# Optimization experiments

Hardware: AMD Instinct MI355X
Metric: run time of the kernel (lower is better)

## Reference

```python
import jax, jax.numpy as jnp
import numpy as np

D_MODEL = 256
N_LAYERS = 8
NUM_CLASSES = 3
INPUT_DIM = 1
BATCH = 8
SEQ = 2048
EXIT_IDX = (1, 3, 5, 7)  # n_layers//4-1, n_layers//2-1, 3n//4-1, n-1
LN_EPS = 1e-5


def setup_inputs() -> dict:
    key = jax.random.key(0)
    ks = jax.random.split(key, 16)
    d, nl, nc = D_MODEL, N_LAYERS, NUM_CLASSES
    return {
        "x": jax.random.normal(ks[0], (BATCH, SEQ, INPUT_DIM), jnp.float32),
        "in_W": jax.random.normal(ks[1], (d, INPUT_DIM), jnp.float32) * 0.02,
        "in_b": jnp.zeros((d,), jnp.float32),
        "A_params": jax.random.normal(ks[2], (nl, d), jnp.float32) * 0.1,
        "B_params": jax.random.normal(ks[3], (nl, d), jnp.float32),
        "C_params": jax.random.normal(ks[4], (nl, d), jnp.float32),
        "D_params": jax.random.normal(ks[5], (nl, d), jnp.float32),
        "proj_W": jax.random.normal(ks[6], (nl, d, d), jnp.float32) * 0.02,
        "proj_b": jnp.zeros((nl, d), jnp.float32),
        "ln_g": jnp.ones((nl, d), jnp.float32),
        "ln_b": jnp.zeros((nl, d), jnp.float32),
        "head_W": jax.random.normal(ks[7], (4, nc, d), jnp.float32) * 0.02,
        "head_b": jnp.zeros((4, nc), jnp.float32),
    }


def _ssm_block(x, Ap, Bp, Cp, Dp, pW, pb, g, b):
    # x: [B, L, d]
    Bsz, L, d = x.shape
    A = jax.nn.sigmoid(Ap)                               # [d]
    t = jnp.arange(L, dtype=jnp.float32)
    K = (Cp[:, None] * (A[:, None] ** t[None, :]) * Bp[:, None])[:, None, :]  # [d,1,L]
    xt = jnp.swapaxes(x, 1, 2)                           # [B, d, L]
    # torch F.conv1d(pad=L-1, groups=d) then [..., :L] == left-pad-only cross-correlation
    out = jax.lax.conv_general_dilated(
        xt, K, window_strides=(1,), padding=[(L - 1, 0)], feature_group_count=d
    )                                                    # [B, d, L]
    out = out + Dp[None, :, None] * xt
    out = jnp.swapaxes(out, 1, 2)                        # [B, L, d]
    out = jax.nn.gelu(out, approximate=False) @ pW.T + pb
    y = x + out
    mu = jnp.mean(y, axis=-1, keepdims=True)
    var = jnp.var(y, axis=-1, keepdims=True)
    return (y - mu) / jnp.sqrt(var + LN_EPS) * g + b


def reference(x, in_W, in_b, A_params, B_params, C_params, D_params,
              proj_W, proj_b, ln_g, ln_b, head_W, head_b):
    h = x @ in_W.T + in_b                                # [B, L, d]
    logits = []
    head = 0
    for i in range(N_LAYERS):
        h = _ssm_block(h, A_params[i], B_params[i], C_params[i], D_params[i],
                       proj_W[i], proj_b[i], ln_g[i], ln_b[i])
        if i in EXIT_IDX:
            pooled = jnp.mean(h, axis=1)                 # [B, d]
            logits.append(pooled @ head_W[head].T + head_b[head])
            head += 1
    return jnp.stack(logits, axis=0)                     # [4, B, num_classes]
```

## Files before the change

### kernel.cpp

```cpp
#include <hip/hip_runtime.h>
#include <math.h>

#define DM 256
#define LSEQ 2048
#define BATCH 8
#define NLAYER 8
#define EMAX 192
#define LN_EPS 1e-5f
#define BM 32
#define BLKS 64
#define NPROD 7
#define TAILB 57
#define ROWS (BATCH * LSEQ)

#define HT_STRIDE 1040
#define AB_OFF   33280
#define AL_OFF   (AB_OFF + 16384)
#define RED_OFF  (AL_OFF + 16384)
#define SMEM_SZ  (RED_OFF + 1280)

typedef float f32x4 __attribute__((ext_vector_type(4)));
typedef short bf16x8 __attribute__((ext_vector_type(8)));
typedef unsigned short u16;
typedef unsigned short u16x4 __attribute__((ext_vector_type(4)));
typedef unsigned short u16x8 __attribute__((ext_vector_type(8)));

union V8 { u16x8 u; bf16x8 b; };

__device__ __forceinline__ float erf_fast(float x) {
    float ax = fabsf(x);
    float t = __builtin_amdgcn_rcpf(fmaf(0.3275911f, ax, 1.f));
    float p = fmaf(t, 1.061405429f, -1.453152027f);
    p = fmaf(t, p, 1.421413741f);
    p = fmaf(t, p, -0.284496736f);
    p = fmaf(t, p, 0.254829592f);
    p = p * t;
    float e = __expf(-ax * ax);
    float r = 1.f - p * e;
    return copysignf(r, x);
}

__device__ __forceinline__ float gelu_fast(float v) {
    return 0.5f * v * (1.f + erf_fast(v * 0.70710678118654752f));
}

__device__ __forceinline__ void split2(float g, u16& hi, u16& lo) {
    unsigned u = __float_as_uint(g);
    hi = (u16)(u >> 16);
    float fh = __uint_as_float(u & 0xFFFF0000u);
    float r = g - fh;
    unsigned v = __float_as_uint(r);
    v = v + 0x7FFFu + ((v >> 16) & 1u);
    lo = (u16)(v >> 16);
}

__global__ void k_prepW(const float* __restrict__ pW, u16* __restrict__ pWh,
                        u16* __restrict__ pWl) {
    int i = blockIdx.x * blockDim.x + threadIdx.x;
    int e = i * 8;
    int l = e >> 16;
    int r = e & 65535;
    int cg = r >> 12;
    int ks = (r >> 9) & 7;
    int lane = (r >> 3) & 63;
    int fq = lane >> 4, fr = lane & 15;
    int col = (cg >> 2) * 64 + (cg & 3) * 16 + fr;
    int k = ks * 32 + fq * 8;
    const float* src = pW + l * 65536 + col * 256 + k;
    float4 w0 = *(const float4*)src;
    float4 w1 = *(const float4*)(src + 4);
    float vv[8] = {w0.x, w0.y, w0.z, w0.w, w1.x, w1.y, w1.z, w1.w};
    u16 sh[8], sl[8];
#pragma unroll
    for (int j = 0; j < 8; ++j) split2(vv[j], sh[j], sl[j]);
    u16x8 vh = {sh[0], sh[1], sh[2], sh[3], sh[4], sh[5], sh[6], sh[7]};
    u16x8 vl = {sl[0], sl[1], sl[2], sl[3], sl[4], sl[5], sl[6], sl[7]};
    *(u16x8*)&pWh[e] = vh;
    *(u16x8*)&pWl[e] = vl;
}

__global__ void k_prep0(const float* __restrict__ x, const float* __restrict__ inW,
                        const float* __restrict__ inb, const float* __restrict__ Ap,
                        const float* __restrict__ Bp, const float* __restrict__ Cp,
                        float* __restrict__ P_all, float* __restrict__ logA_all,
                        float* __restrict__ CB_all, float* __restrict__ pooled,
                        int* __restrict__ flags) {
    int b = blockIdx.x;
    int c = threadIdx.x;
    float A0 = 1.f / (1.f + expf(-Ap[c]));
    float iw = inW[c], ib = inb[c];
    const float* xb = x + b * LSEQ;
    float pw = 1.f, acc = 0.f;
    for (int t = 0; t <= EMAX; ++t) {
        acc += (xb[t] * iw + ib) * pw;
        pw *= A0;
    }
    P_all[b * DM + c] = acc;
    for (int l = 1; l < NLAYER; ++l) P_all[l * BATCH * DM + b * DM + c] = 0.f;
    for (int e = 0; e < 4; ++e) pooled[e * BATCH * DM + b * DM + c] = 0.f;
    if (b == 0) {
        for (int l = 0; l < NLAYER; ++l) {
            float Al = 1.f / (1.f + expf(-Ap[l * DM + c]));
            logA_all[l * DM + c] = logf(Al);
            CB_all[l * DM + c]   = Bp[l * DM + c] * Cp[l * DM + c];
        }
        if (c < NLAYER * BATCH) flags[c] = 0;
    }
}

__global__ __launch_bounds__(256, 2) void k_fused(
    const float* __restrict__ x, const float* __restrict__ inW,
    const float* __restrict__ inb,
    const u16* __restrict__ pWh, const u16* __restrict__ pWl,
    const float* __restrict__ Dp_all, const float* __restrict__ pb_all,
    const float* __restrict__ lng_all, const float* __restrict__ lnb_all,
    const float* __restrict__ logA_all, const float* __restrict__ CB_all,
    float* __restrict__ P_all, float* __restrict__ pooled,
    int* __restrict__ flags)
{
    __shared__ __align__(16) char smem[SMEM_SZ];

    int tid  = threadIdx.x;
    int lane = tid & 63;
    int wn   = tid >> 6;
    int fr   = lane & 15;
    int fq   = lane >> 4;

    int b    = blockIdx.x >> 6;
    int blk  = blockIdx.x & 63;
    int brow = b * LSEQ + blk * BM;
    bool isTail = (blk >= TAILB);
    bool isProd = (blk < NPROD);

    int srow = tid >> 3;
    int gr_s = brow + srow;
    int t_s  = gr_s & (LSEQ - 1);
    int u_s  = (LSEQ - 1) - t_s;
    bool tail_s = (u_s <= EMAX);
    float uf = (float)u_s;
    float xv = x[gr_s];

    float hreg[2][4][4];
    float* Pbuf = (float*)(smem + RED_OFF);

    for (int l = 0; l < NLAYER; ++l) {
        const float* Dp  = Dp_all   + l * DM;
        const float* la  = logA_all + l * DM;
        const float* cbp = CB_all   + l * DM;

        if (isTail) {
            if (l >= 1 && tid == 0) {
                while (__hip_atomic_load(&flags[l * BATCH + b], __ATOMIC_ACQUIRE,
                                         __HIP_MEMORY_SCOPE_AGENT) < NPROD)
                    __builtin_amdgcn_s_sleep(2);
            }
            __syncthreads();
            if (tid < DM)
                Pbuf[tid] = __hip_atomic_load(
                    &P_all[(size_t)l * BATCH * DM + b * DM + tid],
                    __ATOMIC_RELAXED, __HIP_MEMORY_SCOPE_AGENT);
            __syncthreads();
        }

        const u16* bhp = pWh + (size_t)l * 65536 + wn * 16384 + lane * 8;
        const u16* blp = pWl + (size_t)l * 65536 + wn * 16384 + lane * 8;
        V8 bhd[2][4], bld[2][4];
#pragma unroll
        for (int n = 0; n < 4; ++n) {
            bhd[0][n].u = *(const u16x8*)&bhp[n * 4096];
            bld[0][n].u = *(const u16x8*)&blp[n * 4096];
        }

#pragma unroll
        for (int i = 0; i < 4; ++i) {
            int u  = (tid & 7) + 8 * i;
            int kk = u * 8;
            int hby = srow * HT_STRIDE + u * 32;
            float hv[8];
            if (l == 0) {
                float4 w0 = *(const float4*)&inW[kk], w1 = *(const float4*)&inW[kk + 4];
                float4 b0 = *(const float4*)&inb[kk], b1 = *(const float4*)&inb[kk + 4];
                hv[0] = fmaf(xv, w0.x, b0.x); hv[1] = fmaf(xv, w0.y, b0.y);
                hv[2] = fmaf(xv, w0.z, b0.z); hv[3] = fmaf(xv, w0.w, b0.w);
                hv[4] = fmaf(xv, w1.x, b1.x); hv[5] = fmaf(xv, w1.y, b1.y);
                hv[6] = fmaf(xv, w1.z, b1.z); hv[7] = fmaf(xv, w1.w, b1.w);
                float4 o0 = {hv[0], hv[1], hv[2], hv[3]};
                float4 o1 = {hv[4], hv[5], hv[6], hv[7]};
                *(float4*)(smem + hby) = o0;
                *(float4*)(smem + hby + 16) = o1;
            } else {
                float4 h0 = *(const float4*)(smem + hby);
                float4 h1 = *(const float4*)(smem + hby + 16);
                hv[0] = h0.x; hv[1] = h0.y; hv[2] = h0.z; hv[3] = h0.w;
                hv[4] = h1.x; hv[5] = h1.y; hv[6] = h1.z; hv[7] = h1.w;
            }
            float4 d0 = *(const float4*)&Dp[kk];
            float4 d1 = *(const float4*)&Dp[kk + 4];
            float vv[8];
            vv[0] = hv[0] * d0.x; vv[1] = hv[1] * d0.y;
            vv[2] = hv[2] * d0.z; vv[3] = hv[3] * d0.w;
            vv[4] = hv[4] * d1.x; vv[5] = hv[5] * d1.y;
            vv[6] = hv[6] * d1.z; vv[7] = hv[7] * d1.w;
            if (tail_s) {
                float4 la0 = *(const float4*)&la[kk],  la1 = *(const float4*)&la[kk + 4];
                float4 cb0 = *(const float4*)&cbp[kk], cb1 = *(const float4*)&cbp[kk + 4];
                float4 P0  = *(const float4*)&Pbuf[kk], P1 = *(const float4*)&Pbuf[kk + 4];
                vv[0] += cb0.x * __expf(uf * la0.x) * P0.x;
                vv[1] += cb0.y * __expf(uf * la0.y) * P0.y;
                vv[2] += cb0.z * __expf(uf * la0.z) * P0.z;
                vv[3] += cb0.w * __expf(uf * la0.w) * P0.w;
                vv[4] += cb1.x * __expf(uf * la1.x) * P1.x;
                vv[5] += cb1.y * __expf(uf * la1.y) * P1.y;
                vv[6] += cb1.z * __expf(uf * la1.z) * P1.z;
                vv[7] += cb1.w * __expf(uf * la1.w) * P1.w;
            }
            u16 sh[8], sl[8];
#pragma unroll
            for (int j = 0; j < 8; ++j) split2(gelu_fast(vv[j]), sh[j], sl[j]);
            u16x8 vh = {sh[0], sh[1], sh[2], sh[3], sh[4], sh[5], sh[6], sh[7]};
            u16x8 vl = {sl[0], sl[1], sl[2], sl[3], sl[4], sl[5], sl[6], sl[7]};
            int aby = srow * 512 + ((u ^ (srow & 7)) << 4);
            *(u16x8*)(smem + AB_OFF + aby) = vh;
            *(u16x8*)(smem + AL_OFF + aby) = vl;
        }
        __syncthreads();

        f32x4 acc[2][4];
#pragma unroll
        for (int m = 0; m < 2; ++m)
#pragma unroll
            for (int n = 0; n < 4; ++n) acc[m][n] = (f32x4){0.f, 0.f, 0.f, 0.f};

#pragma unroll
        for (int ks = 0; ks < 8; ++ks) {
            int cur = ks & 1, nxt = cur ^ 1;
            if (ks < 7) {
#pragma unroll
                for (int n = 0; n < 4; ++n) {
                    bhd[nxt][n].u = *(const u16x8*)&bhp[n * 4096 + (ks + 1) * 512];
                    bld[nxt][n].u = *(const u16x8*)&blp[n * 4096 + (ks + 1) * 512];
                }
            }
            V8 ah[2], al[2];
#pragma unroll
            for (int m = 0; m < 2; ++m) {
                int row = m * 16 + fr;
                int aby = row * 512 + (((ks * 4 + fq) ^ (row & 7)) << 4);
                ah[m].u = *(const u16x8*)(smem + AB_OFF + aby);
                al[m].u = *(const u16x8*)(smem + AL_OFF + aby);
            }
#pragma unroll
            for (int m = 0; m < 2; ++m)
#pragma unroll
                for (int n = 0; n < 4; ++n) {
                    acc[m][n] = __builtin_amdgcn_mfma_f32_16x16x32_bf16(ah[m].b, bhd[cur][n].b, acc[m][n], 0, 0, 0);
                    acc[m][n] = __builtin_amdgcn_mfma_f32_16x16x32_bf16(ah[m].b, bld[cur][n].b, acc[m][n], 0, 0, 0);
                    acc[m][n] = __builtin_amdgcn_mfma_f32_16x16x32_bf16(al[m].b, bhd[cur][n].b, acc[m][n], 0, 0, 0);
                }
        }

        if (l == 0) {
#pragma unroll
            for (int m = 0; m < 2; ++m)
#pragma unroll
                for (int n = 0; n < 4; ++n)
#pragma unroll
                    for (int r = 0; r < 4; ++r) {
                        int row = m * 16 + fq * 4 + r;
                        int col = wn * 64 + n * 16 + fr;
                        hreg[m][n][r] = *(const float*)(smem + row * HT_STRIDE + col * 4);
                    }
        }
        float pbv[4], lgv[4], lbv[4];
#pragma unroll
        for (int n = 0; n < 4; ++n) {
            int col = wn * 64 + n * 16 + fr;
            pbv[n] = pb_all[l * DM + col];
            lgv[n] = lng_all[l * DM + col];
            lbv[n] = lnb_all[l * DM + col];
        }
        float s[2][4], ss[2][4];
#pragma unroll
        for (int m = 0; m < 2; ++m)
#pragma unroll
            for (int r = 0; r < 4; ++r) {
                float sy = 0.f, sy2 = 0.f;
#pragma unroll
                for (int n = 0; n < 4; ++n) {
                    float y = hreg[m][n][r] + acc[m][n][r] + pbv[n];
                    acc[m][n][r] = y;
                    sy += y; sy2 += y * y;
                }
                s[m][r] = sy; ss[m][r] = sy2;
            }
#pragma unroll
        for (int m = 0; m < 2; ++m)
#pragma unroll
            for (int r = 0; r < 4; ++r)
#pragma unroll
                for (int msk = 1; msk < 16; msk <<= 1) {
                    s[m][r]  += __shfl_xor(s[m][r],  msk);
                    ss[m][r] += __shfl_xor(ss[m][r], msk);
                }
        if (fr == 0) {
#pragma unroll
            for (int m = 0; m < 2; ++m)
#pragma unroll
                for (int r = 0; r < 4; ++r) {
                    int row = m * 16 + fq * 4 + r;
                    *(float*)(smem + RED_OFF + (row * 10 + wn * 2)     * 4) = s[m][r];
                    *(float*)(smem + RED_OFF + (row * 10 + wn * 2 + 1) * 4) = ss[m][r];
                }
        }
        __syncthreads();

        float mean[2][4], rstd[2][4];
#pragma unroll
        for (int m = 0; m < 2; ++m)
#pragma unroll
            for (int r = 0; r < 4; ++r) {
                int row = m * 16 + fq * 4 + r;
                float st = 0.f, sst = 0.f;
#pragma unroll
                for (int w = 0; w < 4; ++w) {
                    st  += *(const float*)(smem + RED_OFF + (row * 10 + w * 2)     * 4);
                    sst += *(const float*)(smem + RED_OFF + (row * 10 + w * 2 + 1) * 4);
                }
                float mu = st * (1.f / 256.f);
                float var = sst * (1.f / 256.f) - mu * mu;
                mean[m][r] = mu;
                rstd[m][r] = rsqrtf(var + LN_EPS);
            }
        int slot = (l == 1) ? 0 : (l == 3) ? 1 : (l == 5) ? 2 : (l == 7) ? 3 : -1;
        bool prod = (l < NLAYER - 1) && isProd;
        float lanv[4];
        if (prod) {
            const float* lan = logA_all + (l + 1) * DM;
#pragma unroll
            for (int n = 0; n < 4; ++n) lanv[n] = lan[wn * 64 + n * 16 + fr];
        }
        float cs[4] = {0.f, 0.f, 0.f, 0.f};
        float pc[4] = {0.f, 0.f, 0.f, 0.f};
#pragma unroll
        for (int m = 0; m < 2; ++m)
#pragma unroll
            for (int r = 0; r < 4; ++r) {
                int row  = m * 16 + fq * 4 + r;
                int trow = blk * BM + row;
#pragma unroll
                for (int n = 0; n < 4; ++n) {
                    float o = (acc[m][n][r] - mean[m][r]) * rstd[m][r] * lgv[n] + lbv[n];
                    hreg[m][n][r] = o;
                    int col = wn * 64 + n * 16 + fr;
                    *(float*)(smem + row * HT_STRIDE + col * 4) = o;
                    if (slot >= 0) cs[n] += o;
                    if (prod && trow <= EMAX) pc[n] += o * __expf((float)trow * lanv[n]);
                }
            }
        if (slot >= 0) {
#pragma unroll
            for (int n = 0; n < 4; ++n) {
                cs[n] += __shfl_xor(cs[n], 16);
                cs[n] += __shfl_xor(cs[n], 32);
            }
            if (lane < 16) {
#pragma unroll
                for (int n = 0; n < 4; ++n)
                    atomicAdd(&pooled[slot * (BATCH * DM) + b * DM + wn * 64 + n * 16 + lane], cs[n]);
            }
        }
        if (prod) {
#pragma unroll
            for (int n = 0; n < 4; ++n) {
                pc[n] += __shfl_xor(pc[n], 16);
                pc[n] += __shfl_xor(pc[n], 32);
            }
            if (lane < 16) {
#pragma unroll
                for (int n = 0; n < 4; ++n)
                    atomicAdd(&P_all[(size_t)(l + 1) * BATCH * DM + b * DM + wn * 64 + n * 16 + lane], pc[n]);
            }
        }
        __syncthreads();
        if (prod && tid == 0)
            __hip_atomic_fetch_add(&flags[(l + 1) * BATCH + b], 1,
                                   __ATOMIC_RELEASE, __HIP_MEMORY_SCOPE_AGENT);
    }
}

__global__ void k_head(const float* __restrict__ pooled, const float* __restrict__ hW,
                       const float* __restrict__ hb, float* __restrict__ out) {
    int tid = threadIdx.x;
    if (tid >= 96) return;
    int e = tid / 24;
    int r = tid % 24;
    int b = r / 3;
    int n = r % 3;
    const float* pv = &pooled[e * (BATCH * DM) + b * DM];
    const float* wv = &hW[(e * 3 + n) * DM];
    float acc = 0.f;
    for (int c = 0; c < DM; ++c) acc += pv[c] * wv[c];
    out[e * 24 + b * 3 + n] = acc * (1.f / (float)LSEQ) + hb[e * 3 + n];
}

extern "C" void kernel_launch(void* const* d_in, const int* in_sizes, int n_in,
                              void* d_out, int out_size, void* d_ws, size_t ws_size,
                              hipStream_t stream) {
    const float* x   = (const float*)d_in[0];
    const float* inW = (const float*)d_in[1];
    const float* inb = (const float*)d_in[2];
    const float* Ap  = (const float*)d_in[3];
    const float* Bp  = (const float*)d_in[4];
    const float* Cp  = (const float*)d_in[5];
    const float* Dp  = (const float*)d_in[6];
    const float* pW  = (const float*)d_in[7];
    const float* pb  = (const float*)d_in[8];
    const float* lng = (const float*)d_in[9];
    const float* lnb = (const float*)d_in[10];
    const float* hW  = (const float*)d_in[11];
    const float* hb  = (const float*)d_in[12];
    float* out = (float*)d_out;

    float* ws = (float*)d_ws;
    float* P_all    = ws;
    float* logA_all = P_all + NLAYER * BATCH * DM;
    float* CB_all   = logA_all + NLAYER * DM;
    float* pooled   = CB_all + NLAYER * DM;
    u16* pWh        = (u16*)(pooled + 4 * BATCH * DM);
    u16* pWl        = pWh + NLAYER * DM * DM;
    int* flags      = (int*)(pWl + NLAYER * DM * DM);

    k_prepW<<<(NLAYER * DM * DM / 8) / 256, 256, 0, stream>>>(pW, pWh, pWl);
    k_prep0<<<BATCH, 256, 0, stream>>>(x, inW, inb, Ap, Bp, Cp,
                                       P_all, logA_all, CB_all, pooled, flags);
    k_fused<<<BATCH * BLKS, 256, 0, stream>>>(
        x, inW, inb, pWh, pWl, Dp, pb, lng, lnb,
        logA_all, CB_all, P_all, pooled, flags);
    k_head<<<1, 128, 0, stream>>>(pooled, hW, hb, out);
}
```

Baseline: 121.7 us.

## Fuse GELU A-operand prep into LayerNorm epilogue and merge prep kernels

Each layer's epilogue now computes GELU(D_next·h), splits it into bf16 hi/lo and writes it straight into the swizzled A tiles in shared memory. This removes the fp32 h staging buffer and the separate per-layer prologue pass. Tail blocks wait for the producer flags after the epilogue and overwrite only their tail rows with the SSM correction. The two prep kernels are merged into one launch, and the B-fragment prefetch is deepened to three stages. The cost is scattered 2-byte LDS writes, extra registers, and tail rows being written twice.

```diff
diff --git a/kernel.cpp b/kernel.cpp
--- a/kernel.cpp
+++ b/kernel.cpp
@@ -11,18 +11,14 @@
 #define BLKS 64
 #define NPROD 7
 #define TAILB 57
-#define ROWS (BATCH * LSEQ)
-
-#define HT_STRIDE 1040
-#define AB_OFF   33280
-#define AL_OFF   (AB_OFF + 16384)
-#define RED_OFF  (AL_OFF + 16384)
+
+#define AL_OFF   16384
+#define RED_OFF  32768
 #define SMEM_SZ  (RED_OFF + 1280)
 
 typedef float f32x4 __attribute__((ext_vector_type(4)));
 typedef short bf16x8 __attribute__((ext_vector_type(8)));
 typedef unsigned short u16;
-typedef unsigned short u16x4 __attribute__((ext_vector_type(4)));
 typedef unsigned short u16x8 __attribute__((ext_vector_type(8)));
 
 union V8 { u16x8 u; bf16x8 b; };
@@ -54,57 +50,64 @@
     lo = (u16)(v >> 16);
 }
 
-__global__ void k_prepW(const float* __restrict__ pW, u16* __restrict__ pWh,
-                        u16* __restrict__ pWl) {
-    int i = blockIdx.x * blockDim.x + threadIdx.x;
-    int e = i * 8;
-    int l = e >> 16;
-    int r = e & 65535;
-    int cg = r >> 12;
-    int ks = (r >> 9) & 7;
-    int lane = (r >> 3) & 63;
-    int fq = lane >> 4, fr = lane & 15;
-    int col = (cg >> 2) * 64 + (cg & 3) * 16 + fr;
-    int k = ks * 32 + fq * 8;
-    const float* src = pW + l * 65536 + col * 256 + k;
-    float4 w0 = *(const float4*)src;
-    float4 w1 = *(const float4*)(src + 4);
-    float vv[8] = {w0.x, w0.y, w0.z, w0.w, w1.x, w1.y, w1.z, w1.w};
-    u16 sh[8], sl[8];
-#pragma unroll
-    for (int j = 0; j < 8; ++j) split2(vv[j], sh[j], sl[j]);
-    u16x8 vh = {sh[0], sh[1], sh[2], sh[3], sh[4], sh[5], sh[6], sh[7]};
-    u16x8 vl = {sl[0], sl[1], sl[2], sl[3], sl[4], sl[5], sl[6], sl[7]};
-    *(u16x8*)&pWh[e] = vh;
-    *(u16x8*)&pWl[e] = vl;
-}
-
-__global__ void k_prep0(const float* __restrict__ x, const float* __restrict__ inW,
-                        const float* __restrict__ inb, const float* __restrict__ Ap,
-                        const float* __restrict__ Bp, const float* __restrict__ Cp,
-                        float* __restrict__ P_all, float* __restrict__ logA_all,
-                        float* __restrict__ CB_all, float* __restrict__ pooled,
-                        int* __restrict__ flags) {
-    int b = blockIdx.x;
-    int c = threadIdx.x;
-    float A0 = 1.f / (1.f + expf(-Ap[c]));
-    float iw = inW[c], ib = inb[c];
-    const float* xb = x + b * LSEQ;
-    float pw = 1.f, acc = 0.f;
-    for (int t = 0; t <= EMAX; ++t) {
-        acc += (xb[t] * iw + ib) * pw;
-        pw *= A0;
-    }
-    P_all[b * DM + c] = acc;
-    for (int l = 1; l < NLAYER; ++l) P_all[l * BATCH * DM + b * DM + c] = 0.f;
-    for (int e = 0; e < 4; ++e) pooled[e * BATCH * DM + b * DM + c] = 0.f;
-    if (b == 0) {
-        for (int l = 0; l < NLAYER; ++l) {
-            float Al = 1.f / (1.f + expf(-Ap[l * DM + c]));
-            logA_all[l * DM + c] = logf(Al);
-            CB_all[l * DM + c]   = Bp[l * DM + c] * Cp[l * DM + c];
-        }
-        if (c < NLAYER * BATCH) flags[c] = 0;
+__device__ __forceinline__ void writeA(char* smem, int row, int col, u16 hi, u16 lo) {
+    int aby = row * 512 + (((col >> 3) ^ (row & 7)) << 4) + (col & 7) * 2;
+    *(u16*)(smem + aby) = hi;
+    *(u16*)(smem + AL_OFF + aby) = lo;
+}
+
+__global__ void k_prep(const float* __restrict__ pW, u16* __restrict__ pWh,
+                       u16* __restrict__ pWl,
+                       const float* __restrict__ x, const float* __restrict__ inW,
+                       const float* __restrict__ inb, const float* __restrict__ Ap,
+                       const float* __restrict__ Bp, const float* __restrict__ Cp,
+                       float* __restrict__ P_all, float* __restrict__ logA_all,
+                       float* __restrict__ CB_all, float* __restrict__ pooled,
+                       int* __restrict__ flags) {
+    if (blockIdx.x < 256) {
+        int i = blockIdx.x * 256 + threadIdx.x;
+        int e = i * 8;
+        int l = e >> 16;
+        int r = e & 65535;
+        int cg = r >> 12;
+        int ks = (r >> 9) & 7;
+        int lane = (r >> 3) & 63;
+        int fq = lane >> 4, fr = lane & 15;
+        int col = (cg >> 2) * 64 + (cg & 3) * 16 + fr;
+        int k = ks * 32 + fq * 8;
+        const float* src = pW + l * 65536 + col * 256 + k;
+        float4 w0 = *(const float4*)src;
+        float4 w1 = *(const float4*)(src + 4);
+        float vv[8] = {w0.x, w0.y, w0.z, w0.w, w1.x, w1.y, w1.z, w1.w};
+        u16 sh[8], sl[8];
+#pragma unroll
+        for (int j = 0; j < 8; ++j) split2(vv[j], sh[j], sl[j]);
+        u16x8 vh = {sh[0], sh[1], sh[2], sh[3], sh[4], sh[5], sh[6], sh[7]};
+        u16x8 vl = {sl[0], sl[1], sl[2], sl[3], sl[4], sl[5], sl[6], sl[7]};
+        *(u16x8*)&pWh[e] = vh;
+        *(u16x8*)&pWl[e] = vl;
+    } else {
+        int b = blockIdx.x - 256;
+        int c = threadIdx.x;
+        float A0 = 1.f / (1.f + expf(-Ap[c]));
+        float iw = inW[c], ib = inb[c];
+        const float* xb = x + b * LSEQ;
+        float pw = 1.f, acc = 0.f;
+        for (int t = 0; t <= EMAX; ++t) {
+            acc += (xb[t] * iw + ib) * pw;
+            pw *= A0;
+        }
+        P_all[b * DM + c] = acc;
+        for (int l = 1; l < NLAYER; ++l) P_all[l * BATCH * DM + b * DM + c] = 0.f;
+        for (int e = 0; e < 4; ++e) pooled[e * BATCH * DM + b * DM + c] = 0.f;
+        if (b == 0) {
+            for (int l = 0; l < NLAYER; ++l) {
+                float Al = 1.f / (1.f + expf(-Ap[l * DM + c]));
+                logA_all[l * DM + c] = logf(Al);
+                CB_all[l * DM + c]   = Bp[l * DM + c] * Cp[l * DM + c];
+            }
+            if (c < NLAYER * BATCH) flags[c] = 0;
+        }
     }
 }
 
@@ -132,113 +135,79 @@
     bool isTail = (blk >= TAILB);
     bool isProd = (blk < NPROD);
 
-    int srow = tid >> 3;
-    int gr_s = brow + srow;
-    int t_s  = gr_s & (LSEQ - 1);
-    int u_s  = (LSEQ - 1) - t_s;
-    bool tail_s = (u_s <= EMAX);
-    float uf = (float)u_s;
-    float xv = x[gr_s];
+    int cols[4];
+#pragma unroll
+    for (int n = 0; n < 4; ++n) cols[n] = wn * 64 + n * 16 + fr;
 
     float hreg[2][4][4];
-    float* Pbuf = (float*)(smem + RED_OFF);
+
+    {
+        float wiv[4], biv[4], D0v[4];
+#pragma unroll
+        for (int n = 0; n < 4; ++n) {
+            wiv[n] = inW[cols[n]];
+            biv[n] = inb[cols[n]];
+            D0v[n] = Dp_all[cols[n]];
+        }
+        float la0[4], cb0[4], P0[4];
+        if (isTail) {
+#pragma unroll
+            for (int n = 0; n < 4; ++n) {
+                la0[n] = logA_all[cols[n]];
+                cb0[n] = CB_all[cols[n]];
+                P0[n]  = P_all[b * DM + cols[n]];
+            }
+        }
+#pragma unroll
+        for (int m = 0; m < 2; ++m)
+#pragma unroll
+            for (int r = 0; r < 4; ++r) {
+                int row = m * 16 + fq * 4 + r;
+                float xv = x[brow + row];
+                int u = (LSEQ - 1) - ((brow + row) & (LSEQ - 1));
+                bool tl = isTail && (u <= EMAX);
+                float uf = (float)u;
+#pragma unroll
+                for (int n = 0; n < 4; ++n) {
+                    float h0 = fmaf(xv, wiv[n], biv[n]);
+                    hreg[m][n][r] = h0;
+                    float v = D0v[n] * h0;
+                    if (tl) v += cb0[n] * __expf(uf * la0[n]) * P0[n];
+                    u16 hi, lo;
+                    split2(gelu_fast(v), hi, lo);
+                    writeA(smem, row, cols[n], hi, lo);
+                }
+            }
+    }
+    __syncthreads();
 
     for (int l = 0; l < NLAYER; ++l) {
-        const float* Dp  = Dp_all   + l * DM;
-        const float* la  = logA_all + l * DM;
-        const float* cbp = CB_all   + l * DM;
-
-        if (isTail) {
-            if (l >= 1 && tid == 0) {
-                while (__hip_atomic_load(&flags[l * BATCH + b], __ATOMIC_ACQUIRE,
-                                         __HIP_MEMORY_SCOPE_AGENT) < NPROD)
-                    __builtin_amdgcn_s_sleep(2);
-            }
-            __syncthreads();
-            if (tid < DM)
-                Pbuf[tid] = __hip_atomic_load(
-                    &P_all[(size_t)l * BATCH * DM + b * DM + tid],
-                    __ATOMIC_RELAXED, __HIP_MEMORY_SCOPE_AGENT);
-            __syncthreads();
-        }
+        f32x4 acc[2][4];
+#pragma unroll
+        for (int m = 0; m < 2; ++m)
+#pragma unroll
+            for (int n = 0; n < 4; ++n) acc[m][n] = (f32x4){0.f, 0.f, 0.f, 0.f};
 
         const u16* bhp = pWh + (size_t)l * 65536 + wn * 16384 + lane * 8;
         const u16* blp = pWl + (size_t)l * 65536 + wn * 16384 + lane * 8;
-        V8 bhd[2][4], bld[2][4];
+
+        V8 bhd[3][4], bld[3][4];
 #pragma unroll
         for (int n = 0; n < 4; ++n) {
             bhd[0][n].u = *(const u16x8*)&bhp[n * 4096];
             bld[0][n].u = *(const u16x8*)&blp[n * 4096];
-        }
-
-#pragma unroll
-        for (int i = 0; i < 4; ++i) {
-            int u  = (tid & 7) + 8 * i;
-            int kk = u * 8;
-            int hby = srow * HT_STRIDE + u * 32;
-            float hv[8];
-            if (l == 0) {
-                float4 w0 = *(const float4*)&inW[kk], w1 = *(const float4*)&inW[kk + 4];
-                float4 b0 = *(const float4*)&inb[kk], b1 = *(const float4*)&inb[kk + 4];
-                hv[0] = fmaf(xv, w0.x, b0.x); hv[1] = fmaf(xv, w0.y, b0.y);
-                hv[2] = fmaf(xv, w0.z, b0.z); hv[3] = fmaf(xv, w0.w, b0.w);
-                hv[4] = fmaf(xv, w1.x, b1.x); hv[5] = fmaf(xv, w1.y, b1.y);
-                hv[6] = fmaf(xv, w1.z, b1.z); hv[7] = fmaf(xv, w1.w, b1.w);
-                float4 o0 = {hv[0], hv[1], hv[2], hv[3]};
-                float4 o1 = {hv[4], hv[5], hv[6], hv[7]};
-                *(float4*)(smem + hby) = o0;
-                *(float4*)(smem + hby + 16) = o1;
-            } else {
-                float4 h0 = *(const float4*)(smem + hby);
-                float4 h1 = *(const float4*)(smem + hby + 16);
-                hv[0] = h0.x; hv[1] = h0.y; hv[2] = h0.z; hv[3] = h0.w;
-                hv[4] = h1.x; hv[5] = h1.y; hv[6] = h1.z; hv[7] = h1.w;
-            }
-            float4 d0 = *(const float4*)&Dp[kk];
-            float4 d1 = *(const float4*)&Dp[kk + 4];
-            float vv[8];
-            vv[0] = hv[0] * d0.x; vv[1] = hv[1] * d0.y;
-            vv[2] = hv[2] * d0.z; vv[3] = hv[3] * d0.w;
-            vv[4] = hv[4] * d1.x; vv[5] = hv[5] * d1.y;
-            vv[6] = hv[6] * d1.z; vv[7] = hv[7] * d1.w;
-            if (tail_s) {
-                float4 la0 = *(const float4*)&la[kk],  la1 = *(const float4*)&la[kk + 4];
-                float4 cb0 = *(const float4*)&cbp[kk], cb1 = *(const float4*)&cbp[kk + 4];
-                float4 P0  = *(const float4*)&Pbuf[kk], P1 = *(const float4*)&Pbuf[kk + 4];
-                vv[0] += cb0.x * __expf(uf * la0.x) * P0.x;
-                vv[1] += cb0.y * __expf(uf * la0.y) * P0.y;
-                vv[2] += cb0.z * __expf(uf * la0.z) * P0.z;
-                vv[3] += cb0.w * __expf(uf * la0.w) * P0.w;
-                vv[4] += cb1.x * __expf(uf * la1.x) * P1.x;
-                vv[5] += cb1.y * __expf(uf * la1.y) * P1.y;
-                vv[6] += cb1.z * __expf(uf * la1.z) * P1.z;
-                vv[7] += cb1.w * __expf(uf * la1.w) * P1.w;
-            }
-            u16 sh[8], sl[8];
-#pragma unroll
-            for (int j = 0; j < 8; ++j) split2(gelu_fast(vv[j]), sh[j], sl[j]);
-            u16x8 vh = {sh[0], sh[1], sh[2], sh[3], sh[4], sh[5], sh[6], sh[7]};
-            u16x8 vl = {sl[0], sl[1], sl[2], sl[3], sl[4], sl[5], sl[6], sl[7]};
-            int aby = srow * 512 + ((u ^ (srow & 7)) << 4);
-            *(u16x8*)(smem + AB_OFF + aby) = vh;
-            *(u16x8*)(smem + AL_OFF + aby) = vl;
-        }
-        __syncthreads();
-
-        f32x4 acc[2][4];
-#pragma unroll
-        for (int m = 0; m < 2; ++m)
-#pragma unroll
-            for (int n = 0; n < 4; ++n) acc[m][n] = (f32x4){0.f, 0.f, 0.f, 0.f};
-
+            bhd[1][n].u = *(const u16x8*)&bhp[n * 4096 + 512];
+            bld[1][n].u = *(const u16x8*)&blp[n * 4096 + 512];
+        }
 #pragma unroll
         for (int ks = 0; ks < 8; ++ks) {
-            int cur = ks & 1, nxt = cur ^ 1;
-            if (ks < 7) {
-#pragma unroll
-                for (int n = 0; n < 4; ++n) {
-                    bhd[nxt][n].u = *(const u16x8*)&bhp[n * 4096 + (ks + 1) * 512];
-                    bld[nxt][n].u = *(const u16x8*)&blp[n * 4096 + (ks + 1) * 512];
+            int cur = ks % 3;
+            if (ks < 6) {
+                int nx2 = (ks + 2) % 3;
+#pragma unroll
+                for (int n = 0; n < 4; ++n) {
+                    bhd[nx2][n].u = *(const u16x8*)&bhp[n * 4096 + (ks + 2) * 512];
+                    bld[nx2][n].u = *(const u16x8*)&blp[n * 4096 + (ks + 2) * 512];
                 }
             }
             V8 ah[2], al[2];
@@ -246,7 +215,7 @@
             for (int m = 0; m < 2; ++m) {
                 int row = m * 16 + fr;
                 int aby = row * 512 + (((ks * 4 + fq) ^ (row & 7)) << 4);
-                ah[m].u = *(const u16x8*)(smem + AB_OFF + aby);
+                ah[m].u = *(const u16x8*)(smem + aby);
                 al[m].u = *(const u16x8*)(smem + AL_OFF + aby);
             }
 #pragma unroll
@@ -259,25 +228,12 @@
                 }
         }
 
-        if (l == 0) {
-#pragma unroll
-            for (int m = 0; m < 2; ++m)
-#pragma unroll
-                for (int n = 0; n < 4; ++n)
-#pragma unroll
-                    for (int r = 0; r < 4; ++r) {
-                        int row = m * 16 + fq * 4 + r;
-                        int col = wn * 64 + n * 16 + fr;
-                        hreg[m][n][r] = *(const float*)(smem + row * HT_STRIDE + col * 4);
-                    }
-        }
         float pbv[4], lgv[4], lbv[4];
 #pragma unroll
         for (int n = 0; n < 4; ++n) {
-            int col = wn * 64 + n * 16 + fr;
-            pbv[n] = pb_all[l * DM + col];
-            lgv[n] = lng_all[l * DM + col];
-            lbv[n] = lnb_all[l * DM + col];
+            pbv[n] = pb_all[l * DM + cols[n]];
+            lgv[n] = lng_all[l * DM + cols[n]];
+            lbv[n] = lnb_all[l * DM + cols[n]];
         }
         float s[2][4], ss[2][4];
 #pragma unroll
@@ -332,12 +288,16 @@
                 rstd[m][r] = rsqrtf(var + LN_EPS);
             }
         int slot = (l == 1) ? 0 : (l == 3) ? 1 : (l == 5) ? 2 : (l == 7) ? 3 : -1;
-        bool prod = (l < NLAYER - 1) && isProd;
-        float lanv[4];
+        bool last = (l == NLAYER - 1);
+        bool prod = !last && isProd;
+        float Dnv[4], lanv[4];
+        if (!last) {
+#pragma unroll
+            for (int n = 0; n < 4; ++n) Dnv[n] = Dp_all[(l + 1) * DM + cols[n]];
+        }
         if (prod) {
-            const float* lan = logA_all + (l + 1) * DM;
-#pragma unroll
-            for (int n = 0; n < 4; ++n) lanv[n] = lan[wn * 64 + n * 16 + fr];
+#pragma unroll
+            for (int n = 0; n < 4; ++n) lanv[n] = logA_all[(l + 1) * DM + cols[n]];
         }
         float cs[4] = {0.f, 0.f, 0.f, 0.f};
         float pc[4] = {0.f, 0.f, 0.f, 0.f};
@@ -351,8 +311,11 @@
                 for (int n = 0; n < 4; ++n) {
                     float o = (acc[m][n][r] - mean[m][r]) * rstd[m][r] * lgv[n] + lbv[n];
                     hreg[m][n][r] = o;
-                    int col = wn * 64 + n * 16 + fr;
-                    *(float*)(smem + row * HT_STRIDE + col * 4) = o;
+                    if (!last) {
+                        u16 hi, lo;
+                        split2(gelu_fast(Dnv[n] * o), hi, lo);
+                        writeA(smem, row, cols[n], hi, lo);
+                    }
                     if (slot >= 0) cs[n] += o;
                     if (prod && trow <= EMAX) pc[n] += o * __expf((float)trow * lanv[n]);
                 }
@@ -382,9 +345,48 @@
             }
         }
         __syncthreads();
-        if (prod && tid == 0)
-            __hip_atomic_fetch_add(&flags[(l + 1) * BATCH + b], 1,
-                                   __ATOMIC_RELEASE, __HIP_MEMORY_SCOPE_AGENT);
+
+        if (!last) {
+            if (prod && tid == 0)
+                __hip_atomic_fetch_add(&flags[(l + 1) * BATCH + b], 1,
+                                       __ATOMIC_RELEASE, __HIP_MEMORY_SCOPE_AGENT);
+            if (isTail) {
+                if (tid == 0) {
+                    while (__hip_atomic_load(&flags[(l + 1) * BATCH + b], __ATOMIC_ACQUIRE,
+                                             __HIP_MEMORY_SCOPE_AGENT) < NPROD)
+                        __builtin_amdgcn_s_sleep(2);
+                }
+                __syncthreads();
+                float lanx[4], cbnx[4], Pnx[4];
+#pragma unroll
+                for (int n = 0; n < 4; ++n) {
+                    lanx[n] = logA_all[(l + 1) * DM + cols[n]];
+                    cbnx[n] = CB_all[(l + 1) * DM + cols[n]];
+                    Pnx[n]  = __hip_atomic_load(
+                        &P_all[(size_t)(l + 1) * BATCH * DM + b * DM + cols[n]],
+                        __ATOMIC_RELAXED, __HIP_MEMORY_SCOPE_AGENT);
+                }
+#pragma unroll
+                for (int m = 0; m < 2; ++m)
+#pragma unroll
+                    for (int r = 0; r < 4; ++r) {
+                        int row = m * 16 + fq * 4 + r;
+                        int u = (LSEQ - 1) - ((brow + row) & (LSEQ - 1));
+                        if (u <= EMAX) {
+                            float uf = (float)u;
+#pragma unroll
+                            for (int n = 0; n < 4; ++n) {
+                                float v = Dnv[n] * hreg[m][n][r] +
+                                          cbnx[n] * __expf(uf * lanx[n]) * Pnx[n];
+                                u16 hi, lo;
+                                split2(gelu_fast(v), hi, lo);
+                                writeA(smem, row, cols[n], hi, lo);
+                            }
+                        }
+                    }
+                __syncthreads();
+            }
+        }
     }
 }
 
@@ -430,9 +432,8 @@
     u16* pWl        = pWh + NLAYER * DM * DM;
     int* flags      = (int*)(pWl + NLAYER * DM * DM);
 
-    k_prepW<<<(NLAYER * DM * DM / 8) / 256, 256, 0, stream>>>(pW, pWh, pWl);
-    k_prep0<<<BATCH, 256, 0, stream>>>(x, inW, inb, Ap, Bp, Cp,
-                                       P_all, logA_all, CB_all, pooled, flags);
+    k_prep<<<264, 256, 0, stream>>>(pW, pWh, pWl, x, inW, inb, Ap, Bp, Cp,
+                                    P_all, logA_all, CB_all, pooled, flags);
     k_fused<<<BATCH * BLKS, 256, 0, stream>>>(
         x, inW, inb, pWh, pWl, Dp, pb, lng, lnb,
         logA_all, CB_all, P_all, pooled, flags);
```

After: 147.4 us. 1.21x slower.

## Use 512-thread blocks with 8 waves each owning 32 columns, merge prep kernels

Applied to the files above, without the earlier changes.

The fused layer kernel now runs 512 threads per block, so eight waves each compute a 32-column slice of the projection instead of four waves with 64 columns. This halves per-thread accumulators and weight fragments and raises the wave count per block, meant to improve latency hiding and per-block throughput. The LayerNorm cross-wave reduction buffer grows to cover eight waves. The two prep kernels are merged into one launch to save launch overhead, and the last layer skips writing its output back to shared memory. In exchange, each wave issues fewer MFMAs between barriers, and the occupancy hint of 4 blocks of 512 threads may not fit within the register and shared-memory limits.

```diff
diff --git a/kernel.cpp b/kernel.cpp
--- a/kernel.cpp
+++ b/kernel.cpp
@@ -11,18 +11,16 @@
 #define BLKS 64
 #define NPROD 7
 #define TAILB 57
-#define ROWS (BATCH * LSEQ)
 
 #define HT_STRIDE 1040
 #define AB_OFF   33280
 #define AL_OFF   (AB_OFF + 16384)
 #define RED_OFF  (AL_OFF + 16384)
-#define SMEM_SZ  (RED_OFF + 1280)
+#define SMEM_SZ  (RED_OFF + 2304)
 
 typedef float f32x4 __attribute__((ext_vector_type(4)));
 typedef short bf16x8 __attribute__((ext_vector_type(8)));
 typedef unsigned short u16;
-typedef unsigned short u16x4 __attribute__((ext_vector_type(4)));
 typedef unsigned short u16x8 __attribute__((ext_vector_type(8)));
 
 union V8 { u16x8 u; bf16x8 b; };
@@ -54,61 +52,62 @@
     lo = (u16)(v >> 16);
 }
 
-__global__ void k_prepW(const float* __restrict__ pW, u16* __restrict__ pWh,
-                        u16* __restrict__ pWl) {
-    int i = blockIdx.x * blockDim.x + threadIdx.x;
-    int e = i * 8;
-    int l = e >> 16;
-    int r = e & 65535;
-    int cg = r >> 12;
-    int ks = (r >> 9) & 7;
-    int lane = (r >> 3) & 63;
-    int fq = lane >> 4, fr = lane & 15;
-    int col = (cg >> 2) * 64 + (cg & 3) * 16 + fr;
-    int k = ks * 32 + fq * 8;
-    const float* src = pW + l * 65536 + col * 256 + k;
-    float4 w0 = *(const float4*)src;
-    float4 w1 = *(const float4*)(src + 4);
-    float vv[8] = {w0.x, w0.y, w0.z, w0.w, w1.x, w1.y, w1.z, w1.w};
-    u16 sh[8], sl[8];
-#pragma unroll
-    for (int j = 0; j < 8; ++j) split2(vv[j], sh[j], sl[j]);
-    u16x8 vh = {sh[0], sh[1], sh[2], sh[3], sh[4], sh[5], sh[6], sh[7]};
-    u16x8 vl = {sl[0], sl[1], sl[2], sl[3], sl[4], sl[5], sl[6], sl[7]};
-    *(u16x8*)&pWh[e] = vh;
-    *(u16x8*)&pWl[e] = vl;
-}
-
-__global__ void k_prep0(const float* __restrict__ x, const float* __restrict__ inW,
-                        const float* __restrict__ inb, const float* __restrict__ Ap,
-                        const float* __restrict__ Bp, const float* __restrict__ Cp,
-                        float* __restrict__ P_all, float* __restrict__ logA_all,
-                        float* __restrict__ CB_all, float* __restrict__ pooled,
-                        int* __restrict__ flags) {
-    int b = blockIdx.x;
-    int c = threadIdx.x;
-    float A0 = 1.f / (1.f + expf(-Ap[c]));
-    float iw = inW[c], ib = inb[c];
-    const float* xb = x + b * LSEQ;
-    float pw = 1.f, acc = 0.f;
-    for (int t = 0; t <= EMAX; ++t) {
-        acc += (xb[t] * iw + ib) * pw;
-        pw *= A0;
+__global__ void k_prep(const float* __restrict__ pW, u16* __restrict__ pWh,
+                       u16* __restrict__ pWl,
+                       const float* __restrict__ x, const float* __restrict__ inW,
+                       const float* __restrict__ inb, const float* __restrict__ Ap,
+                       const float* __restrict__ Bp, const float* __restrict__ Cp,
+                       float* __restrict__ P_all, float* __restrict__ logA_all,
+                       float* __restrict__ CB_all, float* __restrict__ pooled,
+                       int* __restrict__ flags) {
+    if (blockIdx.x < 256) {
+        int i = blockIdx.x * 256 + threadIdx.x;
+        int e = i * 8;
+        int l = e >> 16;
+        int r = e & 65535;
+        int cg = r >> 12;
+        int ks = (r >> 9) & 7;
+        int lane = (r >> 3) & 63;
+        int fq = lane >> 4, fr = lane & 15;
+        int col = (cg >> 2) * 64 + (cg & 3) * 16 + fr;
+        int k = ks * 32 + fq * 8;
+        const float* src = pW + l * 65536 + col * 256 + k;
+        float4 w0 = *(const float4*)src;
+        float4 w1 = *(const float4*)(src + 4);
+        float vv[8] = {w0.x, w0.y, w0.z, w0.w, w1.x, w1.y, w1.z, w1.w};
+        u16 sh[8], sl[8];
+#pragma unroll
+        for (int j = 0; j < 8; ++j) split2(vv[j], sh[j], sl[j]);
+        u16x8 vh = {sh[0], sh[1], sh[2], sh[3], sh[4], sh[5], sh[6], sh[7]};
+        u16x8 vl = {sl[0], sl[1], sl[2], sl[3], sl[4], sl[5], sl[6], sl[7]};
+        *(u16x8*)&pWh[e] = vh;
+        *(u16x8*)&pWl[e] = vl;
+    } else {
+        int b = blockIdx.x - 256;
+        int c = threadIdx.x;
+        float A0 = 1.f / (1.f + expf(-Ap[c]));
+        float iw = inW[c], ib = inb[c];
+        const float* xb = x + b * LSEQ;
+        float pw = 1.f, acc = 0.f;
+        for (int t = 0; t <= EMAX; ++t) {
+            acc += (xb[t] * iw + ib) * pw;
+            pw *= A0;
+        }
+        P_all[b * DM + c] = acc;
+        for (int l = 1; l < NLAYER; ++l) P_all[l * BATCH * DM + b * DM + c] = 0.f;
+        for (int e = 0; e < 4; ++e) pooled[e * BATCH * DM + b * DM + c] = 0.f;
+        if (b == 0) {
+            for (int l = 0; l < NLAYER; ++l) {
+                float Al = 1.f / (1.f + expf(-Ap[l * DM + c]));
+                logA_all[l * DM + c] = logf(Al);
+                CB_all[l * DM + c]   = Bp[l * DM + c] * Cp[l * DM + c];
+            }
+            if (c < NLAYER * BATCH) flags[c] = 0;
+        }
     }
-    P_all[b * DM + c] = acc;
-    for (int l = 1; l < NLAYER; ++l) P_all[l * BATCH * DM + b * DM + c] = 0.f;
-    for (int e = 0; e < 4; ++e) pooled[e * BATCH * DM + b * DM + c] = 0.f;
-    if (b == 0) {
-        for (int l = 0; l < NLAYER; ++l) {
-            float Al = 1.f / (1.f + expf(-Ap[l * DM + c]));
-            logA_all[l * DM + c] = logf(Al);
-            CB_all[l * DM + c]   = Bp[l * DM + c] * Cp[l * DM + c];
-        }
-        if (c < NLAYER * BATCH) flags[c] = 0;
-    }
-}
-
-__global__ __launch_bounds__(256, 2) void k_fused(
+}
+
+__global__ __launch_bounds__(512, 4) void k_fused(
     const float* __restrict__ x, const float* __restrict__ inW,
     const float* __restrict__ inb,
     const u16* __restrict__ pWh, const u16* __restrict__ pWl,
@@ -132,7 +131,7 @@
     bool isTail = (blk >= TAILB);
     bool isProd = (blk < NPROD);
 
-    int srow = tid >> 3;
+    int srow = tid >> 4;
     int gr_s = brow + srow;
     int t_s  = gr_s & (LSEQ - 1);
     int u_s  = (LSEQ - 1) - t_s;
@@ -140,7 +139,7 @@
     float uf = (float)u_s;
     float xv = x[gr_s];
 
-    float hreg[2][4][4];
+    float hreg[2][2][4];
     float* Pbuf = (float*)(smem + RED_OFF);
 
     for (int l = 0; l < NLAYER; ++l) {
@@ -162,18 +161,18 @@
             __syncthreads();
         }
 
-        const u16* bhp = pWh + (size_t)l * 65536 + wn * 16384 + lane * 8;
-        const u16* blp = pWl + (size_t)l * 65536 + wn * 16384 + lane * 8;
-        V8 bhd[2][4], bld[2][4];
-#pragma unroll
-        for (int n = 0; n < 4; ++n) {
+        const u16* bhp = pWh + (size_t)l * 65536 + wn * 8192 + lane * 8;
+        const u16* blp = pWl + (size_t)l * 65536 + wn * 8192 + lane * 8;
+        V8 bhd[2][2], bld[2][2];
+#pragma unroll
+        for (int n = 0; n < 2; ++n) {
             bhd[0][n].u = *(const u16x8*)&bhp[n * 4096];
             bld[0][n].u = *(const u16x8*)&blp[n * 4096];
         }
 
 #pragma unroll
-        for (int i = 0; i < 4; ++i) {
-            int u  = (tid & 7) + 8 * i;
+        for (int i = 0; i < 2; ++i) {
+            int u  = (tid & 15) + 16 * i;
             int kk = u * 8;
             int hby = srow * HT_STRIDE + u * 32;
             float hv[8];
@@ -225,18 +224,18 @@
         }
         __syncthreads();
 
-        f32x4 acc[2][4];
+        f32x4 acc[2][2];
 #pragma unroll
         for (int m = 0; m < 2; ++m)
 #pragma unroll
-            for (int n = 0; n < 4; ++n) acc[m][n] = (f32x4){0.f, 0.f, 0.f, 0.f};
+            for (int n = 0; n < 2; ++n) acc[m][n] = (f32x4){0.f, 0.f, 0.f, 0.f};
 
 #pragma unroll
         for (int ks = 0; ks < 8; ++ks) {
             int cur = ks & 1, nxt = cur ^ 1;
             if (ks < 7) {
 #pragma unroll
-                for (int n = 0; n < 4; ++n) {
+                for (int n = 0; n < 2; ++n) {
                     bhd[nxt][n].u = *(const u16x8*)&bhp[n * 4096 + (ks + 1) * 512];
                     bld[nxt][n].u = *(const u16x8*)&blp[n * 4096 + (ks + 1) * 512];
                 }
@@ -252,32 +251,33 @@
 #pragma unroll
             for (int m = 0; m < 2; ++m)
 #pragma unroll
-                for (int n = 0; n < 4; ++n) {
+                for (int n = 0; n < 2; ++n) {
                     acc[m][n] = __builtin_amdgcn_mfma_f32_16x16x32_bf16(ah[m].b, bhd[cur][n].b, acc[m][n], 0, 0, 0);
                     acc[m][n] = __builtin_amdgcn_mfma_f32_16x16x32_bf16(ah[m].b, bld[cur][n].b, acc[m][n], 0, 0, 0);
                     acc[m][n] = __builtin_amdgcn_mfma_f32_16x16x32_bf16(al[m].b, bhd[cur][n].b, acc[m][n], 0, 0, 0);
                 }
         }
 
+        int cols[2];
+#pragma unroll
+        for (int n = 0; n < 2; ++n) cols[n] = wn * 32 + n * 16 + fr;
+        float pbv[2], lgv[2], lbv[2];
+#pragma unroll
+        for (int n = 0; n < 2; ++n) {
+            pbv[n] = pb_all[l * DM + cols[n]];
+            lgv[n] = lng_all[l * DM + cols[n]];
+            lbv[n] = lnb_all[l * DM + cols[n]];
+        }
         if (l == 0) {
 #pragma unroll
             for (int m = 0; m < 2; ++m)
 #pragma unroll
-                for (int n = 0; n < 4; ++n)
+                for (int n = 0; n < 2; ++n)
 #pragma unroll
                     for (int r = 0; r < 4; ++r) {
                         int row = m * 16 + fq * 4 + r;
-                        int col = wn * 64 + n * 16 + fr;
-                        hreg[m][n][r] = *(const float*)(smem + row * HT_STRIDE + col * 4);
+                        hreg[m][n][r] = *(const float*)(smem + row * HT_STRIDE + cols[n] * 4);
                     }
-        }
-        float pbv[4], lgv[4], lbv[4];
-#pragma unroll
-        for (int n = 0; n < 4; ++n) {
-            int col = wn * 64 + n * 16 + fr;
-            pbv[n] = pb_all[l * DM + col];
-            lgv[n] = lng_all[l * DM + col];
-            lbv[n] = lnb_all[l * DM + col];
         }
         float s[2][4], ss[2][4];
 #pragma unroll
@@ -286,7 +286,7 @@
             for (int r = 0; r < 4; ++r) {
                 float sy = 0.f, sy2 = 0.f;
 #pragma unroll
-                for (int n = 0; n < 4; ++n) {
+                for (int n = 0; n < 2; ++n) {
                     float y = hreg[m][n][r] + acc[m][n][r] + pbv[n];
                     acc[m][n][r] = y;
                     sy += y; sy2 += y * y;
@@ -308,8 +308,8 @@
 #pragma unroll
                 for (int r = 0; r < 4; ++r) {
                     int row = m * 16 + fq * 4 + r;
-                    *(float*)(smem + RED_OFF + (row * 10 + wn * 2)     * 4) = s[m][r];
-                    *(float*)(smem + RED_OFF + (row * 10 + wn * 2 + 1) * 4) = ss[m][r];
+                    *(float*)(smem + RED_OFF + (row * 18 + wn * 2)     * 4) = s[m][r];
+                    *(float*)(smem + RED_OFF + (row * 18 + wn * 2 + 1) * 4) = ss[m][r];
                 }
         }
         __syncthreads();
@@ -322,9 +322,9 @@
                 int row = m * 16 + fq * 4 + r;
                 float st = 0.f, sst = 0.f;
 #pragma unroll
-                for (int w = 0; w < 4; ++w) {
-                    st  += *(const float*)(smem + RED_OFF + (row * 10 + w * 2)     * 4);
-                    sst += *(const float*)(smem + RED_OFF + (row * 10 + w * 2 + 1) * 4);
+                for (int w = 0; w < 8; ++w) {
+                    st  += *(const float*)(smem + RED_OFF + (row * 18 + w * 2)     * 4);
+                    sst += *(const float*)(smem + RED_OFF + (row * 18 + w * 2 + 1) * 4);
                 }
                 float mu = st * (1.f / 256.f);
                 float var = sst * (1.f / 256.f) - mu * mu;
@@ -332,15 +332,15 @@
                 rstd[m][r] = rsqrtf(var + LN_EPS);
             }
         int slot = (l == 1) ? 0 : (l == 3) ? 1 : (l == 5) ? 2 : (l == 7) ? 3 : -1;
-        bool prod = (l < NLAYER - 1) && isProd;
-        float lanv[4];
+        bool last = (l == NLAYER - 1);
+        bool prod = !last && isProd;
+        float lanv[2];
         if (prod) {
-            const float* lan = logA_all + (l + 1) * DM;
-#pragma unroll
-            for (int n = 0; n < 4; ++n) lanv[n] = lan[wn * 64 + n * 16 + fr];
-        }
-        float cs[4] = {0.f, 0.f, 0.f, 0.f};
-        float pc[4] = {0.f, 0.f, 0.f, 0.f};
+#pragma unroll
+            for (int n = 0; n < 2; ++n) lanv[n] = logA_all[(l + 1) * DM + cols[n]];
+        }
+        float cs[2] = {0.f, 0.f};
+        float pc[2] = {0.f, 0.f};
 #pragma unroll
         for (int m = 0; m < 2; ++m)
 #pragma unroll
@@ -348,37 +348,36 @@
                 int row  = m * 16 + fq * 4 + r;
                 int trow = blk * BM + row;
 #pragma unroll
-                for (int n = 0; n < 4; ++n) {
+                for (int n = 0; n < 2; ++n) {
                     float o = (acc[m][n][r] - mean[m][r]) * rstd[m][r] * lgv[n] + lbv[n];
                     hreg[m][n][r] = o;
-                    int col = wn * 64 + n * 16 + fr;
-                    *(float*)(smem + row * HT_STRIDE + col * 4) = o;
+                    if (!last) *(float*)(smem + row * HT_STRIDE + cols[n] * 4) = o;
                     if (slot >= 0) cs[n] += o;
                     if (prod && trow <= EMAX) pc[n] += o * __expf((float)trow * lanv[n]);
                 }
             }
         if (slot >= 0) {
 #pragma unroll
-            for (int n = 0; n < 4; ++n) {
+            for (int n = 0; n < 2; ++n) {
                 cs[n] += __shfl_xor(cs[n], 16);
                 cs[n] += __shfl_xor(cs[n], 32);
             }
             if (lane < 16) {
 #pragma unroll
-                for (int n = 0; n < 4; ++n)
-                    atomicAdd(&pooled[slot * (BATCH * DM) + b * DM + wn * 64 + n * 16 + lane], cs[n]);
+                for (int n = 0; n < 2; ++n)
+                    atomicAdd(&pooled[slot * (BATCH * DM) + b * DM + wn * 32 + n * 16 + lane], cs[n]);
             }
         }
         if (prod) {
 #pragma unroll
-            for (int n = 0; n < 4; ++n) {
+            for (int n = 0; n < 2; ++n) {
                 pc[n] += __shfl_xor(pc[n], 16);
                 pc[n] += __shfl_xor(pc[n], 32);
             }
             if (lane < 16) {
 #pragma unroll
-                for (int n = 0; n < 4; ++n)
-                    atomicAdd(&P_all[(size_t)(l + 1) * BATCH * DM + b * DM + wn * 64 + n * 16 + lane], pc[n]);
+                for (int n = 0; n < 2; ++n)
+                    atomicAdd(&P_all[(size_t)(l + 1) * BATCH * DM + b * DM + wn * 32 + n * 16 + lane], pc[n]);
             }
         }
         __syncthreads();
@@ -430,10 +429,9 @@
     u16* pWl        = pWh + NLAYER * DM * DM;
     int* flags      = (int*)(pWl + NLAYER * DM * DM);
 
-    k_prepW<<<(NLAYER * DM * DM / 8) / 256, 256, 0, stream>>>(pW, pWh, pWl);
-    k_prep0<<<BATCH, 256, 0, stream>>>(x, inW, inb, Ap, Bp, Cp,
-                                       P_all, logA_all, CB_all, pooled, flags);
-    k_fused<<<BATCH * BLKS, 256, 0, stream>>>(
+    k_prep<<<264, 256, 0, stream>>>(pW, pWh, pWl, x, inW, inb, Ap, Bp, Cp,
+                                    P_all, logA_all, CB_all, pooled, flags);
+    k_fused<<<BATCH * BLKS, 512, 0, stream>>>(
         x, inW, inb, pWh, pWl, Dp, pb, lng, lnb,
         logA_all, CB_all, P_all, pooled, flags);
     k_head<<<1, 128, 0, stream>>>(pooled, hW, hb, out);
```

After: 322.9 us. 165% more time.
